# Kernel optimization log

Measured on AMD Instinct MI355X. Metric: run time of the kernel, lower is better.

## Reference

```python
import jax, jax.numpy as jnp
import numpy as np

B, T, D, H, L = 1024, 512, 16, 30, 10


def setup_inputs() -> dict:
    key = jax.random.key(0)
    ks = jax.random.split(key, 8)
    s = 1.0 / np.sqrt(H)  # PyTorch RNN init scale (uniform +-1/sqrt(H)); normal*s is fine for a numeric baseline
    return {
        "x": jax.random.normal(ks[0], (B, T, D), dtype=jnp.float32),
        "W_ih0": jax.random.normal(ks[1], (H, D), dtype=jnp.float32) * s,
        "W_ih": jax.random.normal(ks[2], (L - 1, H, H), dtype=jnp.float32) * s,
        "W_hh": jax.random.normal(ks[3], (L, H, H), dtype=jnp.float32) * s,
        "b_ih": jax.random.normal(ks[4], (L, H), dtype=jnp.float32) * s,
        "b_hh": jax.random.normal(ks[5], (L, H), dtype=jnp.float32) * s,
        "fc_w": jax.random.normal(ks[6], (1, H), dtype=jnp.float32) * s,
        "fc_b": jax.random.normal(ks[7], (1,), dtype=jnp.float32) * s,
    }


def _rnn_layer(x, Wi, Wh, bi, bh):
    # x: [B, T, Din] -> [B, T, H]; h_t = tanh(x_t Wi^T + bi + h_{t-1} Wh^T + bh)
    xw = jnp.einsum("btd,hd->bth", x, Wi) + (bi + bh)  # fold both biases once
    h0 = jnp.zeros((x.shape[0], Wh.shape[0]), dtype=x.dtype)

    def step(h, xw_t):
        h = jnp.tanh(xw_t + h @ Wh.T)
        return h, h

    _, ys = jax.lax.scan(step, h0, jnp.swapaxes(xw, 0, 1))  # scan over time
    return jnp.swapaxes(ys, 0, 1)


def reference(x, W_ih0, W_ih, W_hh, b_ih, b_hh, fc_w, fc_b):
    out = _rnn_layer(x, W_ih0, W_hh[0], b_ih[0], b_hh[0])
    for l in range(1, L):
        out = _rnn_layer(out, W_ih[l - 1], W_hh[l], b_ih[l], b_hh[l])
    # fc on last timestep: [B, H] @ [H, 1] + b -> [B, 1]
    return out[:, -1, :] @ fc_w.T + fc_b
```

## Files before the change

### kernel.cpp

```cpp
#include <hip/hip_runtime.h>

#define TT 512
#define DD 16
#define HH 30
#define LL 10
#define C  4
#define TCH (TT / C)
#define PH (TCH + LL - 1)
#define WRH 40
#define GRP 16
#define BLOCKT (LL * 64)

typedef _Float16 f16x8 __attribute__((ext_vector_type(8)));
typedef float    f32x4 __attribute__((ext_vector_type(4)));

union U128 { uint4 u; f16x8 h; };

#define ACTOFF(par, lm1, cc) ((((par) * (LL - 1) + (lm1)) * C + (cc)) * (GRP * WRH))

__device__ __forceinline__ float tanh_fast(float x) {
    float e = __builtin_amdgcn_exp2f(x * 2.88539008177793f);
    return 1.0f - 2.0f * __builtin_amdgcn_rcpf(e + 1.0f);
}

__device__ __forceinline__ void pipe_barrier() {
    __builtin_amdgcn_sched_barrier(0);
    asm volatile("s_waitcnt lgkmcnt(0)" ::: "memory");
    __builtin_amdgcn_sched_barrier(0);
    __builtin_amdgcn_s_barrier();
    __builtin_amdgcn_sched_barrier(0);
    asm volatile("" ::: "memory");
}

__device__ __forceinline__ int nu_of(int k) {
    return 16 * ((k >> 2) & 1) + 4 * (k >> 3) + (k & 3);
}

__global__ __launch_bounds__(BLOCKT) void rnn_mfma3(
    const float* __restrict__ x,   const float* __restrict__ wi0,
    const float* __restrict__ wih, const float* __restrict__ whh,
    const float* __restrict__ bih, const float* __restrict__ bhh,
    const float* __restrict__ fcw, const float* __restrict__ fcb,
    float* __restrict__ out)
{
    extern __shared__ __align__(16) _Float16 act[];

    const int tid  = threadIdx.x;
    const int l    = tid >> 6;
    const int lane = tid & 63;
    const int n    = lane & 15;
    const int qq   = lane >> 4;
    const int b0   = blockIdx.x * GRP;

    f16x8 wain[2], waown[2];
    #pragma unroll
    for (int tile = 0; tile < 2; ++tile) {
        const int j = 16 * tile + n;
        #pragma unroll
        for (int i = 0; i < 8; ++i) {
            const int kap = 8 * qq + i;
            const int nu  = nu_of(kap);
            float vi = 0.f, vo = 0.f;
            if (j < HH) {
                if (l == 0) { if (kap < DD) vi = wi0[j * DD + kap]; }
                else        { if (nu  < HH) vi = wih[(l - 1) * 900 + j * HH + nu]; }
                if (nu < HH) vo = whh[l * 900 + j * HH + nu];
            }
            wain[tile][i]  = (_Float16)vi;
            waown[tile][i] = (_Float16)vo;
        }
    }
    f32x4 cb[2];
    #pragma unroll
    for (int tile = 0; tile < 2; ++tile)
        #pragma unroll
        for (int r = 0; r < 4; ++r) {
            const int j2 = 16 * tile + 4 * qq + r;
            cb[tile][r] = (j2 < HH) ? bih[l * HH + j2] + bhh[l * HH + j2] : 0.f;
        }
    float fcl[8];
    #pragma unroll
    for (int i = 0; i < 8; ++i) {
        const int nu = nu_of(8 * qq + i);
        fcl[i] = (nu < HH) ? fcw[nu] : 0.f;
    }
    const float fbv = fcb[0];

    float4 xb[C][2];
    const float4* x4 = (const float4*)x;
    const size_t xbase = (size_t)(b0 + n) * TT * 4;
    if (l == 0 && qq < 2) {
        #pragma unroll
        for (int cc = 0; cc < C; ++cc) {
            xb[cc][0] = x4[xbase + cc * 4 + 2 * qq];
            xb[cc][1] = x4[xbase + cc * 4 + 2 * qq + 1];
        }
    }

    f16x8 bown;
    #pragma unroll
    for (int i = 0; i < 8; ++i) bown[i] = (_Float16)0.f;

    __syncthreads();

    for (int p = 0; p < PH; ++p) {
        const int pt = p - l;
        const int q  = (p + 1) & 1;
        const int wp = p & 1;

        if (0 <= pt && pt < TCH) {
            U128 binu[C];
            if (l == 0) {
                #pragma unroll
                for (int cc = 0; cc < C; ++cc) {
                    if (qq < 2) {
                        const float4 u = xb[cc][0], v = xb[cc][1];
                        binu[cc].h[0] = (_Float16)u.x; binu[cc].h[1] = (_Float16)u.y;
                        binu[cc].h[2] = (_Float16)u.z; binu[cc].h[3] = (_Float16)u.w;
                        binu[cc].h[4] = (_Float16)v.x; binu[cc].h[5] = (_Float16)v.y;
                        binu[cc].h[6] = (_Float16)v.z; binu[cc].h[7] = (_Float16)v.w;
                        if (p + 1 < TCH) {
                            const int tn = (p + 1) * C + cc;
                            xb[cc][0] = x4[xbase + tn * 4 + 2 * qq];
                            xb[cc][1] = x4[xbase + tn * 4 + 2 * qq + 1];
                        }
                    } else {
                        binu[cc].u = uint4{0u, 0u, 0u, 0u};
                    }
                }
            } else {
                #pragma unroll
                for (int cc = 0; cc < C; ++cc)
                    binu[cc].u = *(const uint4*)(act + ACTOFF(q, l - 1, cc)
                                                 + n * WRH + 8 * qq);
            }

            f32x4 dp0[C], dp1[C];
            #pragma unroll
            for (int cc = 0; cc < C; ++cc) {
                dp0[cc] = __builtin_amdgcn_mfma_f32_16x16x32_f16(wain[0], binu[cc].h, cb[0], 0, 0, 0);
                dp1[cc] = __builtin_amdgcn_mfma_f32_16x16x32_f16(wain[1], binu[cc].h, cb[1], 0, 0, 0);
            }

            #pragma unroll
            for (int cc = 0; cc < C; ++cc) {
                const f32x4 d0 = __builtin_amdgcn_mfma_f32_16x16x32_f16(waown[0], bown, dp0[cc], 0, 0, 0);
                const f32x4 d1 = __builtin_amdgcn_mfma_f32_16x16x32_f16(waown[1], bown, dp1[cc], 0, 0, 0);
                f16x8 nb;
                #pragma unroll
                for (int r = 0; r < 4; ++r) {
                    nb[r]     = (_Float16)tanh_fast(d0[r]);
                    nb[4 + r] = (_Float16)tanh_fast(d1[r]);
                }
                bown = nb;
                if (l < LL - 1) {
                    U128 w; w.h = nb;
                    *(uint4*)(act + ACTOFF(wp, l, cc) + n * WRH + 8 * qq) = w.u;
                }
            }
        }
        pipe_barrier();
    }

    if (l == LL - 1) {
        float v = 0.f;
        #pragma unroll
        for (int i = 0; i < 8; ++i) v = fmaf((float)bown[i], fcl[i], v);
        v += __shfl_xor(v, 16);
        v += __shfl_xor(v, 32);
        if (qq == 0) out[b0 + n] = v + fbv;
    }
}

extern "C" void kernel_launch(void* const* d_in, const int* in_sizes, int n_in,
                              void* d_out, int out_size, void* d_ws, size_t ws_size,
                              hipStream_t stream) {
    const float* x   = (const float*)d_in[0];
    const float* wi0 = (const float*)d_in[1];
    const float* wih = (const float*)d_in[2];
    const float* whh = (const float*)d_in[3];
    const float* bih = (const float*)d_in[4];
    const float* bhh = (const float*)d_in[5];
    const float* fcw = (const float*)d_in[6];
    const float* fcb = (const float*)d_in[7];
    float* out = (float*)d_out;

    const size_t lds_bytes =
        (size_t)(2 * (LL - 1) * C * GRP * WRH) * sizeof(_Float16);
    hipFuncSetAttribute((const void*)rnn_mfma3,
                        hipFuncAttributeMaxDynamicSharedMemorySize,
                        (int)lds_bytes);

    rnn_mfma3<<<1024 / GRP, BLOCKT, lds_bytes, stream>>>(x, wi0, wih, whh,
                                                         bih, bhh, fcw, fcb, out);
}
```

Baseline: 234.4 us.

## Split RNN layer pipeline across two blocks linked by a global-memory ring

Each batch group's 10-layer wavefront is split over two blocks of 5 layers each instead of one 10-wave block. The first block hands its last layer's outputs to the second through a 4-slot global ring buffer, with spin-wait flags and a credit counter for backpressure. This doubles the number of blocks on the GPU and shortens the skewed pipeline each block runs. It also folds the tanh exp2 prescale into the weights and biases. The cost is cross-block spin-waiting and global-memory latency. Correctness depends on both blocks of a group being resident at the same time, since a block that is not scheduled would deadlock its partner.

After: 335.1 us. 1.43x slower.

```diff
diff --git a/kernel.cpp b/kernel.cpp
--- a/kernel.cpp
+++ b/kernel.cpp
@@ -6,21 +6,25 @@
 #define LL 10
 #define C  4
 #define TCH (TT / C)
-#define PH (TCH + LL - 1)
+#define SKEW 4
+#define PHS (TCH + SKEW)
 #define WRH 40
 #define GRP 16
-#define BLOCKT (LL * 64)
+#define BLOCKT 320
+#define NGRP 64
+#define RING 4
+#define KPRE 2.885390081777927f
 
 typedef _Float16 f16x8 __attribute__((ext_vector_type(8)));
 typedef float    f32x4 __attribute__((ext_vector_type(4)));
 
-union U128 { uint4 u; f16x8 h; };
-
-#define ACTOFF(par, lm1, cc) ((((par) * (LL - 1) + (lm1)) * C + (cc)) * (GRP * WRH))
-
-__device__ __forceinline__ float tanh_fast(float x) {
-    float e = __builtin_amdgcn_exp2f(x * 2.88539008177793f);
-    return 1.0f - 2.0f * __builtin_amdgcn_rcpf(e + 1.0f);
+union U128 { uint4 u; f16x8 h; unsigned long long q[2]; };
+
+#define ACTOFF(par, slot, cc) ((((par) * 4 + (slot)) * C + (cc)) * (GRP * WRH))
+
+__device__ __forceinline__ _Float16 tanh_e(float d) {
+    const float e = __builtin_amdgcn_exp2f(d);
+    return (_Float16)(1.0f - 2.0f * __builtin_amdgcn_rcpf(e + 1.0f));
 }
 
 __device__ __forceinline__ void pipe_barrier() {
@@ -36,21 +40,33 @@
     return 16 * ((k >> 2) & 1) + 4 * (k >> 3) + (k & 3);
 }
 
-__global__ __launch_bounds__(BLOCKT) void rnn_mfma3(
+#define ALOAD(p)    __hip_atomic_load((p),  __ATOMIC_RELAXED, __HIP_MEMORY_SCOPE_AGENT)
+#define ASTORE(p,v) __hip_atomic_store((p), (v), __ATOMIC_RELAXED, __HIP_MEMORY_SCOPE_AGENT)
+
+__global__ __launch_bounds__(BLOCKT) void rnn_stage(
     const float* __restrict__ x,   const float* __restrict__ wi0,
     const float* __restrict__ wih, const float* __restrict__ whh,
     const float* __restrict__ bih, const float* __restrict__ bhh,
     const float* __restrict__ fcw, const float* __restrict__ fcb,
-    float* __restrict__ out)
+    float* __restrict__ out, unsigned* __restrict__ flags,
+    unsigned long long* __restrict__ ring)
 {
-    extern __shared__ __align__(16) _Float16 act[];
-
-    const int tid  = threadIdx.x;
-    const int l    = tid >> 6;
-    const int lane = tid & 63;
-    const int n    = lane & 15;
-    const int qq   = lane >> 4;
-    const int b0   = blockIdx.x * GRP;
+    __shared__ __align__(16) _Float16 act[2 * 4 * C * GRP * WRH];
+
+    const int tid   = threadIdx.x;
+    const int w     = tid >> 6;
+    const int lane  = tid & 63;
+    const int n     = lane & 15;
+    const int qq    = lane >> 4;
+    const int g     = blockIdx.x & (NGRP - 1);
+    const int stage = blockIdx.x >> 6;
+    const int l     = stage * 5 + w;
+    const int b0    = g * GRP;
+
+    unsigned* fl = flags + g;
+    unsigned* cf = flags + NGRP + g;
+    unsigned long long* rg = ring + (size_t)g * (RING * C * GRP * 8);
+#define RIDX(slot, cc) ((((slot) * C + (cc)) * GRP + n) * 8 + qq * 2)
 
     f16x8 wain[2], waown[2];
     #pragma unroll
@@ -66,8 +82,8 @@
                 else        { if (nu  < HH) vi = wih[(l - 1) * 900 + j * HH + nu]; }
                 if (nu < HH) vo = whh[l * 900 + j * HH + nu];
             }
-            wain[tile][i]  = (_Float16)vi;
-            waown[tile][i] = (_Float16)vo;
+            wain[tile][i]  = (_Float16)(vi * KPRE);
+            waown[tile][i] = (_Float16)(vo * KPRE);
         }
     }
     f32x4 cb[2];
@@ -76,7 +92,7 @@
         #pragma unroll
         for (int r = 0; r < 4; ++r) {
             const int j2 = 16 * tile + 4 * qq + r;
-            cb[tile][r] = (j2 < HH) ? bih[l * HH + j2] + bhh[l * HH + j2] : 0.f;
+            cb[tile][r] = (j2 < HH) ? (bih[l * HH + j2] + bhh[l * HH + j2]) * KPRE : 0.f;
         }
     float fcl[8];
     #pragma unroll
@@ -89,7 +105,7 @@
     float4 xb[C][2];
     const float4* x4 = (const float4*)x;
     const size_t xbase = (size_t)(b0 + n) * TT * 4;
-    if (l == 0 && qq < 2) {
+    if (stage == 0 && w == 0 && qq < 2) {
         #pragma unroll
         for (int cc = 0; cc < C; ++cc) {
             xb[cc][0] = x4[xbase + cc * 4 + 2 * qq];
@@ -97,20 +113,36 @@
         }
     }
 
+    U128 rin[C];
+    if (stage == 1 && w == 0) {
+        while ((int)ALOAD(fl) < 1) {}
+        asm volatile("" ::: "memory");
+        #pragma unroll
+        for (int cc = 0; cc < C; ++cc) {
+            rin[cc].q[0] = ALOAD(rg + RIDX(0, cc));
+            rin[cc].q[1] = ALOAD(rg + RIDX(0, cc) + 1);
+        }
+    }
+
     f16x8 bown;
     #pragma unroll
     for (int i = 0; i < 8; ++i) bown[i] = (_Float16)0.f;
 
     __syncthreads();
 
-    for (int p = 0; p < PH; ++p) {
-        const int pt = p - l;
+    for (int p = 0; p < PHS; ++p) {
+        const int pt = p - w;
         const int q  = (p + 1) & 1;
         const int wp = p & 1;
 
         if (0 <= pt && pt < TCH) {
+            if (stage == 0 && w == 4 && pt >= RING) {
+                while ((int)ALOAD(cf) < pt - RING + 1) {}
+                asm volatile("" ::: "memory");
+            }
+
             U128 binu[C];
-            if (l == 0) {
+            if (stage == 0 && w == 0) {
                 #pragma unroll
                 for (int cc = 0; cc < C; ++cc) {
                     if (qq < 2) {
@@ -128,10 +160,23 @@
                         binu[cc].u = uint4{0u, 0u, 0u, 0u};
                     }
                 }
+            } else if (stage == 1 && w == 0) {
+                #pragma unroll
+                for (int cc = 0; cc < C; ++cc) binu[cc] = rin[cc];
+                if (pt + 1 < TCH) {
+                    while ((int)ALOAD(fl) < pt + 2) {}
+                    asm volatile("" ::: "memory");
+                    const int sl = (pt + 1) & (RING - 1);
+                    #pragma unroll
+                    for (int cc = 0; cc < C; ++cc) {
+                        rin[cc].q[0] = ALOAD(rg + RIDX(sl, cc));
+                        rin[cc].q[1] = ALOAD(rg + RIDX(sl, cc) + 1);
+                    }
+                }
             } else {
                 #pragma unroll
                 for (int cc = 0; cc < C; ++cc)
-                    binu[cc].u = *(const uint4*)(act + ACTOFF(q, l - 1, cc)
+                    binu[cc].u = *(const uint4*)(act + ACTOFF(q, w - 1, cc)
                                                  + n * WRH + 8 * qq);
             }
 
@@ -149,20 +194,33 @@
                 f16x8 nb;
                 #pragma unroll
                 for (int r = 0; r < 4; ++r) {
-                    nb[r]     = (_Float16)tanh_fast(d0[r]);
-                    nb[4 + r] = (_Float16)tanh_fast(d1[r]);
+                    nb[r]     = tanh_e(d0[r]);
+                    nb[4 + r] = tanh_e(d1[r]);
                 }
                 bown = nb;
-                if (l < LL - 1) {
-                    U128 w; w.h = nb;
-                    *(uint4*)(act + ACTOFF(wp, l, cc) + n * WRH + 8 * qq) = w.u;
-                }
+                if (w < 4) {
+                    U128 uu; uu.h = nb;
+                    *(uint4*)(act + ACTOFF(wp, w, cc) + n * WRH + 8 * qq) = uu.u;
+                } else if (stage == 0) {
+                    U128 uu; uu.h = nb;
+                    const int sl = pt & (RING - 1);
+                    ASTORE(rg + RIDX(sl, cc),     uu.q[0]);
+                    ASTORE(rg + RIDX(sl, cc) + 1, uu.q[1]);
+                }
+            }
+
+            if (stage == 0 && w == 4) {
+                asm volatile("s_waitcnt vmcnt(0)" ::: "memory");
+                if (lane == 0) ASTORE(fl, (unsigned)(pt + 1));
+            }
+            if (stage == 1 && w == 0) {
+                if (lane == 0) ASTORE(cf, (unsigned)(pt + 1));
             }
         }
         pipe_barrier();
     }
 
-    if (l == LL - 1) {
+    if (stage == 1 && w == 4) {
         float v = 0.f;
         #pragma unroll
         for (int i = 0; i < 8; ++i) v = fmaf((float)bown[i], fcl[i], v);
@@ -185,12 +243,12 @@
     const float* fcb = (const float*)d_in[7];
     float* out = (float*)d_out;
 
-    const size_t lds_bytes =
-        (size_t)(2 * (LL - 1) * C * GRP * WRH) * sizeof(_Float16);
-    hipFuncSetAttribute((const void*)rnn_mfma3,
-                        hipFuncAttributeMaxDynamicSharedMemorySize,
-                        (int)lds_bytes);
-
-    rnn_mfma3<<<1024 / GRP, BLOCKT, lds_bytes, stream>>>(x, wi0, wih, whh,
-                                                         bih, bhh, fcw, fcb, out);
-}
+    unsigned* flags = (unsigned*)d_ws;
+    unsigned long long* ring =
+        (unsigned long long*)((char*)d_ws + 1024);
+
+    hipMemsetAsync(d_ws, 0, 1024, stream);
+
+    rnn_stage<<<2 * NGRP, BLOCKT, 0, stream>>>(x, wi0, wih, whh, bih, bhh,
+                                               fcw, fcb, out, flags, ring);
+}
```
